# Optimization experiments

Hardware: AMD Instinct MI355X
Metric: run time of the kernel (lower is better)

Reference implementation:

```python
import jax, jax.numpy as jnp
import numpy as np

B, T, C, H = 8, 2048, 1024, 128

def setup_inputs() -> dict:
    key = jax.random.key(0)
    k1, k2, k3, k4 = jax.random.split(key, 4)
    scale = C ** -0.5  # init scale for weights, roughly matches nn.Linear default magnitude
    return {
        "x": jax.random.normal(k1, (B, T, C), dtype=jnp.float32),
        "Wk": jax.random.normal(k2, (C, H), dtype=jnp.float32) * scale,
        "Wq": jax.random.normal(k3, (C, H), dtype=jnp.float32) * scale,
        "Wv": jax.random.normal(k4, (C, H), dtype=jnp.float32) * scale,
    }

def reference(x, Wk, Wq, Wv):
    # x: [B, T, C]; W*: [C, H] (torch Linear weight transposed, bias=False)
    Bx, Tx, Cx = x.shape
    k = x @ Wk  # [B, T, H]
    q = x @ Wq  # [B, T, H]
    v = x @ Wv  # [B, T, H]
    # NOTE: original scales by C**(-0.5) (embedding size), not head_size**-0.5
    scores = jnp.einsum('bth,bsh->bts', q, k) * (Cx ** -0.5)  # [B, T, T]
    causal = jnp.tril(jnp.ones((Tx, Tx), dtype=bool))
    scores = jnp.where(causal, scores, -jnp.inf)
    w = jax.nn.softmax(scores, axis=-1)  # dropout is identity in eval mode
    out = jnp.einsum('bts,bsh->bth', w, v)  # [B, T, H]
    return out
```

## Files before the change

kernel.cpp:

```cpp
#include <hip/hip_runtime.h>


typedef __attribute__((ext_vector_type(8))) short short8;
typedef __attribute__((ext_vector_type(4))) float f32x4;

typedef const __attribute__((address_space(1))) unsigned int* gas_u32p;
typedef __attribute__((address_space(3))) unsigned int* las_u32p;

static __device__ __forceinline__ unsigned short f2bf(float f) {
  unsigned int u = __float_as_uint(f);
  u += 0x7FFF + ((u >> 16) & 1);
  return (unsigned short)(u >> 16);
}

__global__ void wtrans_kernel(const float* __restrict__ Wq,
                              const float* __restrict__ Wk,
                              const float* __restrict__ Wv,
                              unsigned short* __restrict__ Wt) {
  int idx = blockIdx.x * blockDim.x + threadIdx.x;
  int C  = idx >> 3;
  int e  = idx & 7;
  int l  = C & 63;
  int t1 = C >> 6;
  int kh = t1 & 1;
  int t2 = t1 >> 1;
  int w  = t2 % 3;
  int t3 = t2 / 3;
  int wave = t3 & 7;
  int kt   = t3 >> 3;
  int n = wave * 16 + (l & 15);
  int k = kt * 64 + kh * 32 + (l >> 4) * 8 + e;
  const float* W = (w == 0) ? Wq : (w == 1) ? Wk : Wv;
  Wt[idx] = f2bf(W[k * 128 + n]);
}

__global__ __launch_bounds__(512) void qkv_kernel(
    const float* __restrict__ x,
    const unsigned short* __restrict__ Wt,
    unsigned short* __restrict__ q,
    unsigned short* __restrict__ kb,
    unsigned short* __restrict__ vt)
{
  __shared__ float xl[3][4096];
  const int tid  = threadIdx.x;
  const int lane = tid & 63;
  const int wave = tid >> 6;
  const int m0   = blockIdx.x * 64;
  const int lr   = lane & 15;

  f32x4 acc[4][3];
  #pragma unroll
  for (int i = 0; i < 4; ++i)
    #pragma unroll
    for (int w = 0; w < 3; ++w) acc[i][w] = (f32x4){0.f, 0.f, 0.f, 0.f};

  int srow[2], skq[2];
  #pragma unroll
  for (int i = 0; i < 2; ++i) {
    int c  = i * 512 + tid;
    int ln = c & 63;
    int g  = c >> 6;
    srow[i] = (g >> 2) * 16 + (ln & 15);
    skq[i]  = ((g >> 1) & 1) * 8 + (ln >> 4) * 2 + (g & 1);
  }

  #define QSTAGE(KT, BUF)                                                        \
    do {                                                                         \
      _Pragma("unroll")                                                          \
      for (int i = 0; i < 2; ++i) {                                              \
        const float* gsrc = x + (size_t)(m0 + srow[i]) * 1024 + (KT) * 64 + skq[i] * 4; \
        __builtin_amdgcn_global_load_lds((gas_u32p)gsrc,                         \
            (las_u32p)&xl[BUF][(i * 512 + tid) * 4], 16, 0, 0);                  \
      }                                                                          \
    } while (0)

  const unsigned short* w2base = Wt + wave * 3072 + lane * 8;

  #define WLOAD(KT, DST)                                                         \
    do {                                                                         \
      _Pragma("unroll")                                                          \
      for (int w = 0; w < 3; ++w) {                                              \
        DST[w][0] = *reinterpret_cast<const short8*>(w2base + (KT) * 24576 + w * 1024);       \
        DST[w][1] = *reinterpret_cast<const short8*>(w2base + (KT) * 24576 + w * 1024 + 512); \
      }                                                                          \
    } while (0)

  short8 wbuf[2][3][2];

  WLOAD(0, wbuf[0]);
  QSTAGE(0, 0);
  QSTAGE(1, 1);

  #pragma unroll
  for (int kt = 0; kt < 16; ++kt) {
    if (kt < 15) WLOAD(kt + 1, wbuf[(kt + 1) & 1]);
    if (kt < 14) QSTAGE(kt + 2, (kt + 2) % 3);
    if (kt < 14)      asm volatile("s_waitcnt vmcnt(10)" ::: "memory");
    else if (kt < 15) asm volatile("s_waitcnt vmcnt(8)"  ::: "memory");
    else              asm volatile("s_waitcnt vmcnt(0)"  ::: "memory");
    __builtin_amdgcn_sched_barrier(0);
    __builtin_amdgcn_s_barrier();

    short8 af[4][2];
    #pragma unroll
    for (int mf = 0; mf < 4; ++mf)
      #pragma unroll
      for (int kh = 0; kh < 2; ++kh) {
        const float* basep = &xl[kt % 3][((mf * 2 + kh) * 2) * 256 + lane * 4];
        f32x4 h0 = *reinterpret_cast<const f32x4*>(basep);
        f32x4 h1 = *reinterpret_cast<const f32x4*>(basep + 256);
        union { unsigned int w[4]; short8 s; } cv;
        asm("v_cvt_pk_bf16_f32 %0, %1, %2" : "=v"(cv.w[0]) : "v"(h0[0]), "v"(h0[1]));
        asm("v_cvt_pk_bf16_f32 %0, %1, %2" : "=v"(cv.w[1]) : "v"(h0[2]), "v"(h0[3]));
        asm("v_cvt_pk_bf16_f32 %0, %1, %2" : "=v"(cv.w[2]) : "v"(h1[0]), "v"(h1[1]));
        asm("v_cvt_pk_bf16_f32 %0, %1, %2" : "=v"(cv.w[3]) : "v"(h1[2]), "v"(h1[3]));
        af[mf][kh] = cv.s;
      }

    __builtin_amdgcn_s_setprio(1);
    #pragma unroll
    for (int w = 0; w < 3; ++w)
      #pragma unroll
      for (int mf = 0; mf < 4; ++mf) {
        acc[mf][w] = __builtin_amdgcn_mfma_f32_16x16x32_bf16(af[mf][0], wbuf[kt & 1][w][0], acc[mf][w], 0, 0, 0);
        acc[mf][w] = __builtin_amdgcn_mfma_f32_16x16x32_bf16(af[mf][1], wbuf[kt & 1][w][1], acc[mf][w], 0, 0, 0);
      }
    __builtin_amdgcn_s_setprio(0);

    asm volatile("s_waitcnt lgkmcnt(0)" ::: "memory");
    __builtin_amdgcn_sched_barrier(0);
    __builtin_amdgcn_s_barrier();
  }
  #undef QSTAGE
  #undef WLOAD

  const int h = wave * 16 + lr;
  const int b = m0 >> 11;
  #pragma unroll
  for (int mf = 0; mf < 4; ++mf) {
    int r0 = m0 + mf * 16 + (lane >> 4) * 4;
    #pragma unroll
    for (int j = 0; j < 4; ++j) {
      int r = r0 + j;
      q[(size_t)r * 128 + h] = f2bf(acc[mf][0][j]);
      int rr  = r & 63;
      int nf  = ((rr >> 5) & 1) * 2 + ((rr >> 2) & 1);
      int lrk = ((rr >> 3) & 3) * 4 + (rr & 3);
      size_t kidx = (size_t)(r >> 6) * 8192
                  + (size_t)(((nf * 4 + (h >> 5)) * 64 + ((h >> 3) & 3) * 16 + lrk) * 8 + (h & 7));
      kb[kidx] = f2bf(acc[mf][1][j]);
    }
    int t = r0 & 2047;
    size_t vidx = (size_t)b * 262144 + (size_t)(t >> 6) * 8192
                + (size_t)(((((h >> 4) * 2 + ((t >> 5) & 1)) * 64 + ((t >> 3) & 3) * 16 + (h & 15)) * 8) + (t & 7));
    ushort4 u;
    u.x = f2bf(acc[mf][2][0]); u.y = f2bf(acc[mf][2][1]);
    u.z = f2bf(acc[mf][2][2]); u.w = f2bf(acc[mf][2][3]);
    *reinterpret_cast<ushort4*>(vt + vidx) = u;
  }
}

template<bool MASK>
static __device__ __forceinline__ void body32(
    int s, int myrow, int lg, int lane,
    const unsigned short* __restrict__ klc,
    const unsigned short* __restrict__ vlc,
    const short8 (&qf)[4], f32x4 (&o)[8], float& lsum)
{
  const float SC = 0.03125f * 1.44269504f;

  short8 kf[2][4];
  #pragma unroll
  for (int nf = 0; nf < 2; ++nf)
    #pragma unroll
    for (int ks = 0; ks < 4; ++ks)
      kf[nf][ks] = *reinterpret_cast<const short8*>(klc + ((nf * 4 + ks) * 64 + lane) * 8);

  f32x4 sT[2];
  __builtin_amdgcn_s_setprio(1);
  #pragma unroll
  for (int nf = 0; nf < 2; ++nf) {
    sT[nf] = (f32x4){0.f, 0.f, 0.f, 0.f};
    #pragma unroll
    for (int ks = 0; ks < 4; ++ks)
      sT[nf] = __builtin_amdgcn_mfma_f32_16x16x32_bf16(kf[nf][ks], qf[ks], sT[nf], 0, 0, 0);
  }
  __builtin_amdgcn_s_setprio(0);

  short8 vf[8];
  #pragma unroll
  for (int n = 0; n < 8; ++n)
    vf[n] = *reinterpret_cast<const short8*>(vlc + (n * 64 + lane) * 8);

  float p[8];
  #pragma unroll
  for (int nf = 0; nf < 2; ++nf)
    #pragma unroll
    for (int j = 0; j < 4; ++j) {
      float sv = sT[nf][j] * SC;
      if (MASK) {
        int kv = s * 32 + lg * 8 + nf * 4 + j;
        if (kv > myrow) sv = -1e30f;
      }
      p[nf * 4 + j] = exp2f(sv);
    }
  lsum += ((p[0] + p[1]) + (p[2] + p[3])) + ((p[4] + p[5]) + (p[6] + p[7]));

  union { unsigned int w[4]; short8 s8; } cv;
  #pragma unroll
  for (int u = 0; u < 4; ++u)
    asm("v_cvt_pk_bf16_f32 %0, %1, %2" : "=v"(cv.w[u]) : "v"(p[u * 2]), "v"(p[u * 2 + 1]));

  __builtin_amdgcn_s_setprio(1);
  #pragma unroll
  for (int n = 0; n < 8; ++n)
    o[n] = __builtin_amdgcn_mfma_f32_16x16x32_bf16(vf[n], cv.s8, o[n], 0, 0, 0);
  __builtin_amdgcn_s_setprio(0);
}

__global__ __launch_bounds__(128) void attn_kernel(
    const unsigned short* __restrict__ q,
    const unsigned short* __restrict__ kb,
    const unsigned short* __restrict__ vt,
    float* __restrict__ out)
{
  __shared__ unsigned short sb[2][2][2][4096];

  const int tid  = threadIdx.x;
  const int lane = tid & 63;
  const int wv   = tid >> 6;
  const int lr = lane & 15;
  const int lg = lane >> 4;
  const int bid = blockIdx.x;
  const int b  = bid & 7;
  const int tt = 127 - (bid >> 3);
  const int t0 = tt * 16;
  const int nb = (tt >> 1) + 1;

  const unsigned short* kbase = kb + (size_t)b * 262144;
  const unsigned short* vbase = vt + (size_t)b * 262144;
  const int myrow = t0 + lr;

  short8 qf[4];
  const unsigned short* qp = q + ((size_t)(b * 2048) + myrow) * 128 + lg * 8;
  #pragma unroll
  for (int ks = 0; ks < 4; ++ks)
    qf[ks] = *reinterpret_cast<const short8*>(qp + ks * 32);

  f32x4 o[8];
  #pragma unroll
  for (int n = 0; n < 8; ++n) o[n] = (f32x4){0.f, 0.f, 0.f, 0.f};
  float lsum = 0.f;

  #define STAGE32(S, BUF)                                                        \
    do {                                                                         \
      const int blk = (S) >> 1, hh = (S) & 1;                                    \
      const unsigned short* kg = kbase + (size_t)blk * 8192 + hh * 4096;         \
      const unsigned short* vg = vbase + (size_t)blk * 8192;                     \
      _Pragma("unroll")                                                          \
      for (int i = 0; i < 8; ++i)                                                \
        __builtin_amdgcn_global_load_lds((gas_u32p)(kg + (i * 64 + lane) * 8),   \
            (las_u32p)&sb[wv][BUF][0][(i * 64 + lane) * 8], 16, 0, 0);           \
      _Pragma("unroll")                                                          \
      for (int i = 0; i < 8; ++i)                                                \
        __builtin_amdgcn_global_load_lds((gas_u32p)(vg + ((i * 2 + hh) * 64 + lane) * 8), \
            (las_u32p)&sb[wv][BUF][1][(i * 64 + lane) * 8], 16, 0, 0);           \
      } while (0)

  if (wv < nb) STAGE32(wv, 0);

  #pragma unroll 1
  for (int s = wv; s < nb; s += 2) {
    const int bufi = (s >> 1) & 1;
    if (s + 2 < nb) {
      STAGE32(s + 2, bufi ^ 1);
      asm volatile("s_waitcnt vmcnt(16)" ::: "memory");
    } else {
      asm volatile("s_waitcnt vmcnt(0)" ::: "memory");
    }
    __builtin_amdgcn_sched_barrier(0);
    if (s == nb - 1)
      body32<true >(s, myrow, lg, lane, sb[wv][bufi][0], sb[wv][bufi][1], qf, o, lsum);
    else
      body32<false>(s, myrow, lg, lane, sb[wv][bufi][0], sb[wv][bufi][1], qf, o, lsum);
  }
  #undef STAGE32

  __syncthreads();
  float* mb = (float*)&sb[1][0][0][0];
  if (wv == 1) {
    #pragma unroll
    for (int n = 0; n < 8; ++n) {
      float4 st;
      st.x = o[n][0]; st.y = o[n][1]; st.z = o[n][2]; st.w = o[n][3];
      *reinterpret_cast<float4*>(&mb[lane * 32 + n * 4]) = st;
    }
    mb[2048 + lane] = lsum;
  }
  __syncthreads();
  if (wv == 0) {
    #pragma unroll
    for (int n = 0; n < 8; ++n) {
      float4 ad = *reinterpret_cast<const float4*>(&mb[lane * 32 + n * 4]);
      o[n][0] += ad.x; o[n][1] += ad.y; o[n][2] += ad.z; o[n][3] += ad.w;
    }
    float ps = lsum + mb[2048 + lane];
    ps += __shfl_xor(ps, 16);
    ps += __shfl_xor(ps, 32);
    float rcp = 1.0f / ps;
    float* op = out + ((size_t)(b * 2048) + myrow) * 128;
    #pragma unroll
    for (int n = 0; n < 8; ++n) {
      float4 st;
      st.x = o[n][0] * rcp; st.y = o[n][1] * rcp;
      st.z = o[n][2] * rcp; st.w = o[n][3] * rcp;
      *reinterpret_cast<float4*>(op + n * 16 + lg * 4) = st;
    }
  }
}

extern "C" void kernel_launch(void* const* d_in, const int* in_sizes, int n_in,
                              void* d_out, int out_size, void* d_ws, size_t ws_size,
                              hipStream_t stream) {
  const float* x  = (const float*)d_in[0];
  const float* Wk = (const float*)d_in[1];
  const float* Wq = (const float*)d_in[2];
  const float* Wv = (const float*)d_in[3];
  float* out = (float*)d_out;

  char* ws = (char*)d_ws;
  unsigned short* q  = (unsigned short*)(ws);
  unsigned short* kb = (unsigned short*)(ws + (4u  << 20));
  unsigned short* vt = (unsigned short*)(ws + (8u  << 20));
  unsigned short* Wt = (unsigned short*)(ws + (12u << 20));

  wtrans_kernel<<<dim3(1536), dim3(256), 0, stream>>>(Wq, Wk, Wv, Wt);
  qkv_kernel<<<dim3(256), dim3(512), 0, stream>>>(x, Wt, q, kb, vt);
  attn_kernel<<<dim3(1024), dim3(128), 0, stream>>>(q, kb, vt, out);
}
```

Measured before the change: 68.19 us.

## Process two query row groups per attention block and quad-buffer QKV staging

The attention kernel now gives each block 32 query rows as two 16-row groups that share every K/V tile loaded into LDS. This halves the grid and the K/V traffic per query row, at the cost of more registers and fewer blocks for latency hiding. The QKV projection kernel moves to a 4-deep LDS ring for x tiles, which lets it drop the trailing wait and barrier in each k-iteration. That second barrier guarded against the next prefetch overwriting a buffer still being read, so the deeper ring has to cover that hazard instead.

```diff
diff --git a/kernel.cpp b/kernel.cpp
--- a/kernel.cpp
+++ b/kernel.cpp
@@ -41,7 +41,7 @@
     unsigned short* __restrict__ kb,
     unsigned short* __restrict__ vt)
 {
-  __shared__ float xl[3][4096];
+  __shared__ float xl[4][4096];
   const int tid  = threadIdx.x;
   const int lane = tid & 63;
   const int wave = tid >> 6;
@@ -94,7 +94,7 @@
   #pragma unroll
   for (int kt = 0; kt < 16; ++kt) {
     if (kt < 15) WLOAD(kt + 1, wbuf[(kt + 1) & 1]);
-    if (kt < 14) QSTAGE(kt + 2, (kt + 2) % 3);
+    if (kt < 14) QSTAGE(kt + 2, (kt + 2) & 3);
     if (kt < 14)      asm volatile("s_waitcnt vmcnt(10)" ::: "memory");
     else if (kt < 15) asm volatile("s_waitcnt vmcnt(8)"  ::: "memory");
     else              asm volatile("s_waitcnt vmcnt(0)"  ::: "memory");
@@ -106,7 +106,7 @@
     for (int mf = 0; mf < 4; ++mf)
       #pragma unroll
       for (int kh = 0; kh < 2; ++kh) {
-        const float* basep = &xl[kt % 3][((mf * 2 + kh) * 2) * 256 + lane * 4];
+        const float* basep = &xl[kt & 3][((mf * 2 + kh) * 2) * 256 + lane * 4];
         f32x4 h0 = *reinterpret_cast<const f32x4*>(basep);
         f32x4 h1 = *reinterpret_cast<const f32x4*>(basep + 256);
         union { unsigned int w[4]; short8 s; } cv;
@@ -126,10 +126,6 @@
         acc[mf][w] = __builtin_amdgcn_mfma_f32_16x16x32_bf16(af[mf][1], wbuf[kt & 1][w][1], acc[mf][w], 0, 0, 0);
       }
     __builtin_amdgcn_s_setprio(0);
-
-    asm volatile("s_waitcnt lgkmcnt(0)" ::: "memory");
-    __builtin_amdgcn_sched_barrier(0);
-    __builtin_amdgcn_s_barrier();
   }
   #undef QSTAGE
   #undef WLOAD
@@ -162,10 +158,10 @@
 
 template<bool MASK>
 static __device__ __forceinline__ void body32(
-    int s, int myrow, int lg, int lane,
+    int s, int myrow0, int myrow1, int lg, int lane,
     const unsigned short* __restrict__ klc,
     const unsigned short* __restrict__ vlc,
-    const short8 (&qf)[4], f32x4 (&o)[8], float& lsum)
+    const short8 (&qf)[2][4], f32x4 (&o)[2][8], float (&lsum)[2])
 {
   const float SC = 0.03125f * 1.44269504f;
 
@@ -176,15 +172,17 @@
     for (int ks = 0; ks < 4; ++ks)
       kf[nf][ks] = *reinterpret_cast<const short8*>(klc + ((nf * 4 + ks) * 64 + lane) * 8);
 
-  f32x4 sT[2];
+  f32x4 sT[2][2];
   __builtin_amdgcn_s_setprio(1);
   #pragma unroll
-  for (int nf = 0; nf < 2; ++nf) {
-    sT[nf] = (f32x4){0.f, 0.f, 0.f, 0.f};
-    #pragma unroll
-    for (int ks = 0; ks < 4; ++ks)
-      sT[nf] = __builtin_amdgcn_mfma_f32_16x16x32_bf16(kf[nf][ks], qf[ks], sT[nf], 0, 0, 0);
-  }
+  for (int g = 0; g < 2; ++g)
+    #pragma unroll
+    for (int nf = 0; nf < 2; ++nf) {
+      sT[g][nf] = (f32x4){0.f, 0.f, 0.f, 0.f};
+      #pragma unroll
+      for (int ks = 0; ks < 4; ++ks)
+        sT[g][nf] = __builtin_amdgcn_mfma_f32_16x16x32_bf16(kf[nf][ks], qf[g][ks], sT[g][nf], 0, 0, 0);
+    }
   __builtin_amdgcn_s_setprio(0);
 
   short8 vf[8];
@@ -192,29 +190,34 @@
   for (int n = 0; n < 8; ++n)
     vf[n] = *reinterpret_cast<const short8*>(vlc + (n * 64 + lane) * 8);
 
-  float p[8];
-  #pragma unroll
-  for (int nf = 0; nf < 2; ++nf)
-    #pragma unroll
-    for (int j = 0; j < 4; ++j) {
-      float sv = sT[nf][j] * SC;
-      if (MASK) {
-        int kv = s * 32 + lg * 8 + nf * 4 + j;
-        if (kv > myrow) sv = -1e30f;
-      }
-      p[nf * 4 + j] = exp2f(sv);
-    }
-  lsum += ((p[0] + p[1]) + (p[2] + p[3])) + ((p[4] + p[5]) + (p[6] + p[7]));
-
-  union { unsigned int w[4]; short8 s8; } cv;
-  #pragma unroll
-  for (int u = 0; u < 4; ++u)
-    asm("v_cvt_pk_bf16_f32 %0, %1, %2" : "=v"(cv.w[u]) : "v"(p[u * 2]), "v"(p[u * 2 + 1]));
+  union { unsigned int w[4]; short8 s8; } cv[2];
+  #pragma unroll
+  for (int g = 0; g < 2; ++g) {
+    const int myrow = g ? myrow1 : myrow0;
+    float p[8];
+    #pragma unroll
+    for (int nf = 0; nf < 2; ++nf)
+      #pragma unroll
+      for (int j = 0; j < 4; ++j) {
+        float sv = sT[g][nf][j] * SC;
+        if (MASK) {
+          int kv = s * 32 + lg * 8 + nf * 4 + j;
+          if (kv > myrow) sv = -1e30f;
+        }
+        p[nf * 4 + j] = exp2f(sv);
+      }
+    lsum[g] += ((p[0] + p[1]) + (p[2] + p[3])) + ((p[4] + p[5]) + (p[6] + p[7]));
+    #pragma unroll
+    for (int u = 0; u < 4; ++u)
+      asm("v_cvt_pk_bf16_f32 %0, %1, %2" : "=v"(cv[g].w[u]) : "v"(p[u * 2]), "v"(p[u * 2 + 1]));
+  }
 
   __builtin_amdgcn_s_setprio(1);
   #pragma unroll
-  for (int n = 0; n < 8; ++n)
-    o[n] = __builtin_amdgcn_mfma_f32_16x16x32_bf16(vf[n], cv.s8, o[n], 0, 0, 0);
+  for (int g = 0; g < 2; ++g)
+    #pragma unroll
+    for (int n = 0; n < 8; ++n)
+      o[g][n] = __builtin_amdgcn_mfma_f32_16x16x32_bf16(vf[n], cv[g].s8, o[g][n], 0, 0, 0);
   __builtin_amdgcn_s_setprio(0);
 }
 
@@ -233,24 +236,30 @@
   const int lg = lane >> 4;
   const int bid = blockIdx.x;
   const int b  = bid & 7;
-  const int tt = 127 - (bid >> 3);
-  const int t0 = tt * 16;
-  const int nb = (tt >> 1) + 1;
+  const int tt = 63 - (bid >> 3);
+  const int t0 = tt * 32;
+  const int nb = tt + 1;
 
   const unsigned short* kbase = kb + (size_t)b * 262144;
   const unsigned short* vbase = vt + (size_t)b * 262144;
-  const int myrow = t0 + lr;
-
-  short8 qf[4];
-  const unsigned short* qp = q + ((size_t)(b * 2048) + myrow) * 128 + lg * 8;
-  #pragma unroll
-  for (int ks = 0; ks < 4; ++ks)
-    qf[ks] = *reinterpret_cast<const short8*>(qp + ks * 32);
-
-  f32x4 o[8];
-  #pragma unroll
-  for (int n = 0; n < 8; ++n) o[n] = (f32x4){0.f, 0.f, 0.f, 0.f};
-  float lsum = 0.f;
+  const int myrow0 = t0 + lr;
+  const int myrow1 = t0 + 16 + lr;
+
+  short8 qf[2][4];
+  #pragma unroll
+  for (int g = 0; g < 2; ++g) {
+    const unsigned short* qp = q + ((size_t)(b * 2048) + (g ? myrow1 : myrow0)) * 128 + lg * 8;
+    #pragma unroll
+    for (int ks = 0; ks < 4; ++ks)
+      qf[g][ks] = *reinterpret_cast<const short8*>(qp + ks * 32);
+  }
+
+  f32x4 o[2][8];
+  #pragma unroll
+  for (int g = 0; g < 2; ++g)
+    #pragma unroll
+    for (int n = 0; n < 8; ++n) o[g][n] = (f32x4){0.f, 0.f, 0.f, 0.f};
+  float lsum[2] = {0.f, 0.f};
 
   #define STAGE32(S, BUF)                                                        \
     do {                                                                         \
@@ -280,9 +289,9 @@
     }
     __builtin_amdgcn_sched_barrier(0);
     if (s == nb - 1)
-      body32<true >(s, myrow, lg, lane, sb[wv][bufi][0], sb[wv][bufi][1], qf, o, lsum);
+      body32<true >(s, myrow0, myrow1, lg, lane, sb[wv][bufi][0], sb[wv][bufi][1], qf, o, lsum);
     else
-      body32<false>(s, myrow, lg, lane, sb[wv][bufi][0], sb[wv][bufi][1], qf, o, lsum);
+      body32<false>(s, myrow0, myrow1, lg, lane, sb[wv][bufi][0], sb[wv][bufi][1], qf, o, lsum);
   }
   #undef STAGE32
 
@@ -290,31 +299,37 @@
   float* mb = (float*)&sb[1][0][0][0];
   if (wv == 1) {
     #pragma unroll
-    for (int n = 0; n < 8; ++n) {
-      float4 st;
-      st.x = o[n][0]; st.y = o[n][1]; st.z = o[n][2]; st.w = o[n][3];
-      *reinterpret_cast<float4*>(&mb[lane * 32 + n * 4]) = st;
-    }
-    mb[2048 + lane] = lsum;
+    for (int g = 0; g < 2; ++g)
+      #pragma unroll
+      for (int n = 0; n < 8; ++n) {
+        float4 st;
+        st.x = o[g][n][0]; st.y = o[g][n][1]; st.z = o[g][n][2]; st.w = o[g][n][3];
+        *reinterpret_cast<float4*>(&mb[(size_t)lane * 64 + g * 32 + n * 4]) = st;
+      }
+    mb[4096 + lane]      = lsum[0];
+    mb[4096 + 64 + lane] = lsum[1];
   }
   __syncthreads();
   if (wv == 0) {
     #pragma unroll
-    for (int n = 0; n < 8; ++n) {
-      float4 ad = *reinterpret_cast<const float4*>(&mb[lane * 32 + n * 4]);
-      o[n][0] += ad.x; o[n][1] += ad.y; o[n][2] += ad.z; o[n][3] += ad.w;
-    }
-    float ps = lsum + mb[2048 + lane];
-    ps += __shfl_xor(ps, 16);
-    ps += __shfl_xor(ps, 32);
-    float rcp = 1.0f / ps;
-    float* op = out + ((size_t)(b * 2048) + myrow) * 128;
-    #pragma unroll
-    for (int n = 0; n < 8; ++n) {
-      float4 st;
-      st.x = o[n][0] * rcp; st.y = o[n][1] * rcp;
-      st.z = o[n][2] * rcp; st.w = o[n][3] * rcp;
-      *reinterpret_cast<float4*>(op + n * 16 + lg * 4) = st;
+    for (int g = 0; g < 2; ++g) {
+      #pragma unroll
+      for (int n = 0; n < 8; ++n) {
+        float4 ad = *reinterpret_cast<const float4*>(&mb[(size_t)lane * 64 + g * 32 + n * 4]);
+        o[g][n][0] += ad.x; o[g][n][1] += ad.y; o[g][n][2] += ad.z; o[g][n][3] += ad.w;
+      }
+      float ps = lsum[g] + mb[4096 + g * 64 + lane];
+      ps += __shfl_xor(ps, 16);
+      ps += __shfl_xor(ps, 32);
+      float rcp = 1.0f / ps;
+      float* op = out + ((size_t)(b * 2048) + (g ? myrow1 : myrow0)) * 128;
+      #pragma unroll
+      for (int n = 0; n < 8; ++n) {
+        float4 st;
+        st.x = o[g][n][0] * rcp; st.y = o[g][n][1] * rcp;
+        st.z = o[g][n][2] * rcp; st.w = o[g][n][3] * rcp;
+        *reinterpret_cast<float4*>(op + n * 16 + lg * 4) = st;
+      }
     }
   }
 }
@@ -336,5 +351,5 @@
 
   wtrans_kernel<<<dim3(1536), dim3(256), 0, stream>>>(Wq, Wk, Wv, Wt);
   qkv_kernel<<<dim3(256), dim3(512), 0, stream>>>(x, Wt, q, kb, vt);
-  attn_kernel<<<dim3(1024), dim3(128), 0, stream>>>(q, kb, vt, out);
-}
+  attn_kernel<<<dim3(512), dim3(128), 0, stream>>>(q, kb, vt, out);
+}
```

Result: slower. 73.77 us (+8.2%).
